# Optimization experiments

Measured on AMD Instinct MI355X. Metric: run time of the kernel, lower is better.

## Reference

```python
import jax, jax.numpy as jnp
import numpy as np
import math

HEAD_DEPTH = 16
CLIP = 10.0
NEG_INF = 1.0e10
# combined scale: (1/sqrt(head_depth)) * log_50(400)
SCALE = (math.log(400.0) / math.log(50.0)) / math.sqrt(HEAD_DEPTH)


def setup_inputs() -> dict:
    key = jax.random.key(0)
    kq, kk, kv, km = jax.random.split(key, 4)
    B, H, S, D = 4, 8, 2048, HEAD_DEPTH
    Q = jax.random.normal(kq, (B, H, S, D), dtype=jnp.float32)
    K = jax.random.normal(kk, (B, H, S, D), dtype=jnp.float32)
    V = jax.random.normal(kv, (B, H, S, D), dtype=jnp.float32)
    # mask: (B, n_nodes, 1) bool; True -> masked (logit set to -inf)
    mask = jax.random.randint(km, (B, S, 1), 0, 2) == 1
    return {"Q": Q, "K": K, "V": V, "mask": mask}


def reference(Q, K, V, mask):
    # logits: (B, H, q_seq, k_seq)
    logits = jnp.einsum("bhqd,bhkd->bhqk", Q, K) * SCALE
    logits = CLIP * jnp.tanh(logits)  # tanh clip
    # mask[:, None, None, :, 0] -> (B, 1, 1, k_seq), True gets -inf
    m = mask[:, None, None, :, 0]
    logits = jnp.where(m, -NEG_INF, logits)
    probs = jax.nn.softmax(logits, axis=-1)
    return jnp.einsum("bhqk,bhkd->bhqd", probs, V)
```

## Files before the change

kernel.cpp:

```cpp
#include <hip/hip_runtime.h>


typedef __fp16 h2 __attribute__((ext_vector_type(2)));
typedef __fp16 h4 __attribute__((ext_vector_type(4)));
typedef float  f4 __attribute__((ext_vector_type(4)));

#define SEQ 2048
#define NBH 32
#define TPB 128
#define KWS_BYTES ((size_t)NBH * TPB * 64 * 8)
#define VWS_BYTES KWS_BYTES
#define BIAS_BYTES ((size_t)4 * SEQ * 4)
#define IDX_BYTES  ((size_t)4 * SEQ * 4)
#define META_BYTES 64
#define WS_NEEDED (KWS_BYTES + VWS_BYTES + BIAS_BYTES + IDX_BYTES + META_BYTES)

__device__ __forceinline__ float fast_exp2(float x) {
#if __has_builtin(__builtin_amdgcn_exp2f)
    return __builtin_amdgcn_exp2f(x);
#else
    return exp2f(x);
#endif
}

__device__ __forceinline__ float dot2acc(h2 a, float accv) {
#if __has_builtin(__builtin_amdgcn_fdot2)
    const h2 one = {(__fp16)1.0f, (__fp16)1.0f};
    return __builtin_amdgcn_fdot2(a, one, accv, false);
#else
    return accv + (float)a[0] + (float)a[1];
#endif
}

__global__ __launch_bounds__(256) void attn_scan(
    const int* __restrict__ maskp, int* __restrict__ idxws,
    float* __restrict__ biasws, int* __restrict__ meta)
{
    __shared__ int partial[256];
    const int b   = blockIdx.x;
    const int tid = threadIdx.x;

    int keep[8], cnt = 0;
    #pragma unroll
    for (int j = 0; j < 8; ++j) {
        keep[j] = (maskp[b * SEQ + tid * 8 + j] == 0);
        cnt += keep[j];
    }
    partial[tid] = cnt;
    __syncthreads();
    for (int off = 1; off < 256; off <<= 1) {
        int add = (tid >= off) ? partial[tid - off] : 0;
        __syncthreads();
        partial[tid] += add;
        __syncthreads();
    }
    const int total = partial[255];
    int pos = partial[tid] - cnt;
    #pragma unroll
    for (int j = 0; j < 8; ++j) {
        if (keep[j]) idxws[b * SEQ + pos++] = tid * 8 + j;
    }
    for (int i = tid; i < SEQ; i += 256) {
        biasws[b * SEQ + i] = (i < total) ? 0.0f : -1.0e30f;
        if (i >= total) idxws[b * SEQ + i] = 0;
    }
    if (tid == 0) {
        int nr = (total + 255) >> 8;
        meta[b] = nr < 1 ? 1 : nr;
    }
}

__global__ __launch_bounds__(256) void attn_prep(
    const float* __restrict__ Kp, const float* __restrict__ Vp,
    const int* __restrict__ idxws,
    __fp16* __restrict__ Kws, __fp16* __restrict__ Vws)
{
    const int tid = threadIdx.x;
    const int T   = blockIdx.x * 4 + (tid >> 6);
    const int l   = tid & 63;
    const int bh  = T >> 7;
    const int t   = T & (TPB - 1);
    const int b   = bh >> 3;
    const int c   = l & 15;
    const int g   = l >> 4;
    const size_t base = (size_t)bh * (SEQ * 16);
    const int*   idx  = idxws + (size_t)b * SEQ;

    {
        const int krow = idx[t * 16 + c];
        f4 kv = *(const f4*)(Kp + base + (size_t)krow * 16 + 4 * g);
        h2 k0 = __builtin_amdgcn_cvt_pkrtz(kv[0], kv[1]);
        h2 k1 = __builtin_amdgcn_cvt_pkrtz(kv[2], kv[3]);
        h4 kh; kh[0] = k0[0]; kh[1] = k0[1]; kh[2] = k1[0]; kh[3] = k1[1];
        *(h4*)(Kws + ((size_t)T * 64 + l) * 4) = kh;
    }
    {
        const int v0 = idx[t * 16 + 4 * g + 0];
        const int v1 = idx[t * 16 + 4 * g + 1];
        const int v2 = idx[t * 16 + 4 * g + 2];
        const int v3 = idx[t * 16 + 4 * g + 3];
        h2 p0 = __builtin_amdgcn_cvt_pkrtz(Vp[base + (size_t)v0 * 16 + c],
                                           Vp[base + (size_t)v1 * 16 + c]);
        h2 p1 = __builtin_amdgcn_cvt_pkrtz(Vp[base + (size_t)v2 * 16 + c],
                                           Vp[base + (size_t)v3 * 16 + c]);
        h4 vh; vh[0] = p0[0]; vh[1] = p0[1]; vh[2] = p1[0]; vh[3] = p1[1];
        *(h4*)(Vws + ((size_t)T * 64 + l) * 4) = vh;
    }
}

__global__ __launch_bounds__(512, 8) void attn_v5(
    const float* __restrict__ Qp, const __fp16* __restrict__ Kws,
    const __fp16* __restrict__ Vws, const float* __restrict__ biasws,
    const int* __restrict__ meta, float* __restrict__ out)
{
    __shared__ __align__(16) _Float16 Kbuf[2][4096];
    __shared__ __align__(16) _Float16 Vbuf[2][4096];
    __shared__ __align__(16) float    Bbuf[2][256];

    const int bid  = blockIdx.x;
    const int bh   = bid >> 5;
    const int qblk = bid & 31;
    const int b    = bh >> 3;
    const int tid  = threadIdx.x;
    const int wave = tid >> 6;
    const int lane = tid & 63;
    const int qt   = wave & 3;
    const int kg   = wave >> 2;
    const int c    = lane & 15;
    const int g    = lane >> 4;

    const size_t base  = (size_t)bh * (SEQ * 16);
    const int    qbase = qblk * 64 + qt * 16;
    const float  c1 = 1.1047809f;
    const float  c2 = -28.8539008f;

    const int nr = meta[b];

    h4 qfrag;
    {
        f4 qv = *(const f4*)(Qp + base + (size_t)(qbase + c) * 16 + 4 * g);
        h2 lo = __builtin_amdgcn_cvt_pkrtz(c1 * qv[0], c1 * qv[1]);
        h2 hi = __builtin_amdgcn_cvt_pkrtz(c1 * qv[2], c1 * qv[3]);
        qfrag[0] = lo[0]; qfrag[1] = lo[1]; qfrag[2] = hi[0]; qfrag[3] = hi[1];
    }

    const f4* ksrc = (const f4*)(Kws + (size_t)bh * TPB * 256);
    const f4* vsrc = (const f4*)(Vws + (size_t)bh * TPB * 256);
    const float* bsrc = biasws + (size_t)b * SEQ;

    f4 kpre = ksrc[tid];
    f4 vpre = vsrc[tid];
    float bpre = (tid < 256) ? bsrc[tid] : 0.0f;
    *(f4*)&Kbuf[0][tid * 8] = kpre;
    *(f4*)&Vbuf[0][tid * 8] = vpre;
    if (tid < 256) Bbuf[0][tid] = bpre;
    {
        const int r1 = (1 < nr) ? 1 : (nr - 1);
        kpre = ksrc[r1 * 512 + tid];
        vpre = vsrc[r1 * 512 + tid];
        if (tid < 256) bpre = bsrc[r1 * 256 + tid];
    }
    __syncthreads();

    f4 acc = {0.f, 0.f, 0.f, 0.f};
    float dsum = 0.f;

    for (int r = 0; r < nr; ++r) {
        const int cb = r & 1, nb = cb ^ 1;
        if (r + 1 < nr) {
            *(f4*)&Kbuf[nb][tid * 8] = kpre;
            *(f4*)&Vbuf[nb][tid * 8] = vpre;
            if (tid < 256) Bbuf[nb][tid] = bpre;
        }
        if (r + 2 < nr) {
            kpre = ksrc[(r + 2) * 512 + tid];
            vpre = vsrc[(r + 2) * 512 + tid];
            if (tid < 256) bpre = bsrc[(r + 2) * 256 + tid];
        }

        const _Float16* Kc = &Kbuf[cb][kg * 2048];
        const _Float16* Vc = &Vbuf[cb][kg * 2048];
        const float*    Bc = &Bbuf[cb][kg * 128];

        #pragma unroll
        for (int t = 0; t < 8; ++t) {
            h4 afrag = *(const h4*)(Kc + t * 256 + lane * 4);
            f4 s = __builtin_amdgcn_mfma_f32_16x16x16f16(
                afrag, qfrag, (f4){0.f, 0.f, 0.f, 0.f}, 0, 0, 0);

            f4 b4 = *(const f4*)(Bc + t * 16 + 4 * g);
            float p[4];
            #pragma unroll
            for (int i = 0; i < 4; ++i) {
                float tt = fast_exp2(s[i]);
                float w  = __builtin_amdgcn_rcpf(1.0f + tt);
                p[i] = fast_exp2(__builtin_fmaf(c2, w, b4[i]));
            }
            h2 plo = __builtin_amdgcn_cvt_pkrtz(p[0], p[1]);
            h2 phi = __builtin_amdgcn_cvt_pkrtz(p[2], p[3]);
            dsum = dot2acc(plo, dsum);
            dsum = dot2acc(phi, dsum);
            h4 pf; pf[0] = plo[0]; pf[1] = plo[1]; pf[2] = phi[0]; pf[3] = phi[1];

            h4 vfrag = *(const h4*)(Vc + t * 256 + lane * 4);
            acc = __builtin_amdgcn_mfma_f32_16x16x16f16(pf, vfrag, acc, 0, 0, 0);
        }
        __syncthreads();
    }

    dsum += __shfl_xor(dsum, 16);
    dsum += __shfl_xor(dsum, 32);

    float* ex = (float*)&Kbuf[0][0];
    const int slot = (qt * 64 + lane) * 5;
    if (kg == 1) {
        ex[slot + 0] = acc[0]; ex[slot + 1] = acc[1];
        ex[slot + 2] = acc[2]; ex[slot + 3] = acc[3];
        ex[slot + 4] = dsum;
    }
    __syncthreads();
    if (kg == 0) {
        const float dT = dsum + ex[slot + 4];
        #pragma unroll
        for (int i = 0; i < 4; ++i) {
            const float denom = __shfl(dT, 4 * g + i);
            out[base + (size_t)(qbase + 4 * g + i) * 16 + c] =
                (acc[i] + ex[slot + i]) / denom;
        }
    }
}

#define KROW 20
#define VROW 520

__global__ __launch_bounds__(512, 8) void attn_fwd_v3(
    const float* __restrict__ Qp, const float* __restrict__ Kp,
    const float* __restrict__ Vp, const int* __restrict__ maskp,
    float* __restrict__ out)
{
    __shared__ __align__(16) _Float16 Klds[512 * KROW];
    __shared__ __align__(16) _Float16 Vt[16 * VROW];
    __shared__ __align__(16) float biasf[512];

    const int bid  = blockIdx.x;
    const int bh   = bid >> 5;
    const int qblk = bid & 31;
    const int b    = bh >> 3;
    const int tid  = threadIdx.x;
    const int wave = tid >> 6;
    const int lane = tid & 63;
    const int qt   = wave & 3;
    const int kg   = wave >> 2;
    const int c    = lane & 15;
    const int g    = lane >> 4;

    const size_t base = (size_t)bh * (SEQ * 16);
    const int qbase = qblk * 64 + qt * 16;
    const float c1 = 1.1047809f;
    const float c2 = -28.8539008f;

    h4 qfrag;
    {
        f4 qv = *(const f4*)(Qp + base + (size_t)(qbase + c) * 16 + 4 * g);
        h2 lo = __builtin_amdgcn_cvt_pkrtz(c1 * qv[0], c1 * qv[1]);
        h2 hi = __builtin_amdgcn_cvt_pkrtz(c1 * qv[2], c1 * qv[3]);
        qfrag[0] = lo[0]; qfrag[1] = lo[1]; qfrag[2] = hi[0]; qfrag[3] = hi[1];
    }

    f4 acc = {0.f, 0.f, 0.f, 0.f};
    float dsum = 0.f;
    const int kgb = kg * 256;

    for (int round = 0; round < 4; ++round) {
        {
            const float* Kc = Kp + base + (size_t)round * (512 * 16);
            const float* Vc = Vp + base + (size_t)round * (512 * 16);
            #pragma unroll
            for (int j = 0; j < 4; ++j) {
                const int i = j * 512 + tid;
                f4 kv = *(const f4*)(Kc + (size_t)i * 4);
                f4 vv = *(const f4*)(Vc + (size_t)i * 4);
                const int key = i >> 2;
                const int dq  = (i & 3) * 4;
                h2 k0 = __builtin_amdgcn_cvt_pkrtz(kv[0], kv[1]);
                h2 k1 = __builtin_amdgcn_cvt_pkrtz(kv[2], kv[3]);
                h4 kh; kh[0] = k0[0]; kh[1] = k0[1]; kh[2] = k1[0]; kh[3] = k1[1];
                *(h4*)&Klds[key * KROW + dq] = kh;
                #pragma unroll
                for (int e = 0; e < 4; ++e)
                    Vt[(dq + e) * VROW + key] = (_Float16)vv[e];
            }
            biasf[tid] = maskp[(size_t)b * SEQ + round * 512 + tid] ? -60.0f : 0.0f;
        }
        __syncthreads();

        #pragma unroll
        for (int t = 0; t < 16; ++t) {
            const int kb = kgb + t * 16;
            h4 afrag = *(const h4*)&Klds[(kb + c) * KROW + 4 * g];
            f4 s = __builtin_amdgcn_mfma_f32_16x16x16f16(
                afrag, qfrag, (f4){0.f, 0.f, 0.f, 0.f}, 0, 0, 0);
            f4 b4 = *(const f4*)&biasf[kb + 4 * g];
            float p[4];
            #pragma unroll
            for (int i = 0; i < 4; ++i) {
                float tt = fast_exp2(s[i]);
                float w  = __builtin_amdgcn_rcpf(1.0f + tt);
                p[i] = fast_exp2(__builtin_fmaf(c2, w, b4[i]));
            }
            h2 plo = __builtin_amdgcn_cvt_pkrtz(p[0], p[1]);
            h2 phi = __builtin_amdgcn_cvt_pkrtz(p[2], p[3]);
            dsum = dot2acc(plo, dsum);
            dsum = dot2acc(phi, dsum);
            h4 pf; pf[0] = plo[0]; pf[1] = plo[1]; pf[2] = phi[0]; pf[3] = phi[1];
            h4 vfrag = *(const h4*)&Vt[c * VROW + kb + 4 * g];
            acc = __builtin_amdgcn_mfma_f32_16x16x16f16(pf, vfrag, acc, 0, 0, 0);
        }
        __syncthreads();
    }

    dsum += __shfl_xor(dsum, 16);
    dsum += __shfl_xor(dsum, 32);

    float* ex = (float*)Klds;
    const int slot = (qt * 64 + lane) * 5;
    if (kg == 1) {
        ex[slot + 0] = acc[0]; ex[slot + 1] = acc[1];
        ex[slot + 2] = acc[2]; ex[slot + 3] = acc[3];
        ex[slot + 4] = dsum;
    }
    __syncthreads();
    if (kg == 0) {
        const float dT = dsum + ex[slot + 4];
        #pragma unroll
        for (int i = 0; i < 4; ++i) {
            const float denom = __shfl(dT, 4 * g + i);
            out[base + (size_t)(qbase + 4 * g + i) * 16 + c] =
                (acc[i] + ex[slot + i]) / denom;
        }
    }
}

extern "C" void kernel_launch(void* const* d_in, const int* in_sizes, int n_in,
                              void* d_out, int out_size, void* d_ws, size_t ws_size,
                              hipStream_t stream) {
    const float* Q    = (const float*)d_in[0];
    const float* K    = (const float*)d_in[1];
    const float* V    = (const float*)d_in[2];
    const int*   mask = (const int*)d_in[3];
    float* out = (float*)d_out;

    if (ws_size >= WS_NEEDED) {
        char* p = (char*)d_ws;
        __fp16* Kws = (__fp16*)p;                       p += KWS_BYTES;
        __fp16* Vws = (__fp16*)p;                       p += VWS_BYTES;
        float*  Bws = (float*)p;                        p += BIAS_BYTES;
        int*    Iws = (int*)p;                          p += IDX_BYTES;
        int*    Mws = (int*)p;
        attn_scan<<<dim3(4), dim3(256), 0, stream>>>(mask, Iws, Bws, Mws);
        attn_prep<<<dim3(1024), dim3(256), 0, stream>>>(K, V, Iws, Kws, Vws);
        attn_v5<<<dim3(1024), dim3(512), 0, stream>>>(Q, Kws, Vws, Bws, Mws, out);
    } else {
        attn_fwd_v3<<<dim3(1024), dim3(512), 0, stream>>>(Q, K, V, mask, out);
    }
}
```

Baseline: 92.77 us.

## Fuse mask compaction and K/V gather into single attention kernel

```diff
diff --git a/kernel.cpp b/kernel.cpp
--- a/kernel.cpp
+++ b/kernel.cpp
@@ -4,16 +4,9 @@
 typedef __fp16 h2 __attribute__((ext_vector_type(2)));
 typedef __fp16 h4 __attribute__((ext_vector_type(4)));
 typedef float  f4 __attribute__((ext_vector_type(4)));
+typedef unsigned short us4 __attribute__((ext_vector_type(4)));
 
 #define SEQ 2048
-#define NBH 32
-#define TPB 128
-#define KWS_BYTES ((size_t)NBH * TPB * 64 * 8)
-#define VWS_BYTES KWS_BYTES
-#define BIAS_BYTES ((size_t)4 * SEQ * 4)
-#define IDX_BYTES  ((size_t)4 * SEQ * 4)
-#define META_BYTES 64
-#define WS_NEEDED (KWS_BYTES + VWS_BYTES + BIAS_BYTES + IDX_BYTES + META_BYTES)
 
 __device__ __forceinline__ float fast_exp2(float x) {
 #if __has_builtin(__builtin_amdgcn_exp2f)
@@ -32,90 +25,15 @@
 #endif
 }
 
-__global__ __launch_bounds__(256) void attn_scan(
-    const int* __restrict__ maskp, int* __restrict__ idxws,
-    float* __restrict__ biasws, int* __restrict__ meta)
-{
-    __shared__ int partial[256];
-    const int b   = blockIdx.x;
-    const int tid = threadIdx.x;
-
-    int keep[8], cnt = 0;
-    #pragma unroll
-    for (int j = 0; j < 8; ++j) {
-        keep[j] = (maskp[b * SEQ + tid * 8 + j] == 0);
-        cnt += keep[j];
-    }
-    partial[tid] = cnt;
-    __syncthreads();
-    for (int off = 1; off < 256; off <<= 1) {
-        int add = (tid >= off) ? partial[tid - off] : 0;
-        __syncthreads();
-        partial[tid] += add;
-        __syncthreads();
-    }
-    const int total = partial[255];
-    int pos = partial[tid] - cnt;
-    #pragma unroll
-    for (int j = 0; j < 8; ++j) {
-        if (keep[j]) idxws[b * SEQ + pos++] = tid * 8 + j;
-    }
-    for (int i = tid; i < SEQ; i += 256) {
-        biasws[b * SEQ + i] = (i < total) ? 0.0f : -1.0e30f;
-        if (i >= total) idxws[b * SEQ + i] = 0;
-    }
-    if (tid == 0) {
-        int nr = (total + 255) >> 8;
-        meta[b] = nr < 1 ? 1 : nr;
-    }
-}
-
-__global__ __launch_bounds__(256) void attn_prep(
-    const float* __restrict__ Kp, const float* __restrict__ Vp,
-    const int* __restrict__ idxws,
-    __fp16* __restrict__ Kws, __fp16* __restrict__ Vws)
-{
-    const int tid = threadIdx.x;
-    const int T   = blockIdx.x * 4 + (tid >> 6);
-    const int l   = tid & 63;
-    const int bh  = T >> 7;
-    const int t   = T & (TPB - 1);
-    const int b   = bh >> 3;
-    const int c   = l & 15;
-    const int g   = l >> 4;
-    const size_t base = (size_t)bh * (SEQ * 16);
-    const int*   idx  = idxws + (size_t)b * SEQ;
-
-    {
-        const int krow = idx[t * 16 + c];
-        f4 kv = *(const f4*)(Kp + base + (size_t)krow * 16 + 4 * g);
-        h2 k0 = __builtin_amdgcn_cvt_pkrtz(kv[0], kv[1]);
-        h2 k1 = __builtin_amdgcn_cvt_pkrtz(kv[2], kv[3]);
-        h4 kh; kh[0] = k0[0]; kh[1] = k0[1]; kh[2] = k1[0]; kh[3] = k1[1];
-        *(h4*)(Kws + ((size_t)T * 64 + l) * 4) = kh;
-    }
-    {
-        const int v0 = idx[t * 16 + 4 * g + 0];
-        const int v1 = idx[t * 16 + 4 * g + 1];
-        const int v2 = idx[t * 16 + 4 * g + 2];
-        const int v3 = idx[t * 16 + 4 * g + 3];
-        h2 p0 = __builtin_amdgcn_cvt_pkrtz(Vp[base + (size_t)v0 * 16 + c],
-                                           Vp[base + (size_t)v1 * 16 + c]);
-        h2 p1 = __builtin_amdgcn_cvt_pkrtz(Vp[base + (size_t)v2 * 16 + c],
-                                           Vp[base + (size_t)v3 * 16 + c]);
-        h4 vh; vh[0] = p0[0]; vh[1] = p0[1]; vh[2] = p1[0]; vh[3] = p1[1];
-        *(h4*)(Vws + ((size_t)T * 64 + l) * 4) = vh;
-    }
-}
-
-__global__ __launch_bounds__(512, 8) void attn_v5(
-    const float* __restrict__ Qp, const __fp16* __restrict__ Kws,
-    const __fp16* __restrict__ Vws, const float* __restrict__ biasws,
-    const int* __restrict__ meta, float* __restrict__ out)
+__global__ __launch_bounds__(512, 8) void attn_fused(
+    const float* __restrict__ Qp, const float* __restrict__ Kp,
+    const float* __restrict__ Vp, const int* __restrict__ maskp,
+    float* __restrict__ out)
 {
     __shared__ __align__(16) _Float16 Kbuf[2][4096];
     __shared__ __align__(16) _Float16 Vbuf[2][4096];
-    __shared__ __align__(16) float    Bbuf[2][256];
+    __shared__ __align__(16) unsigned short idx16[SEQ];
+    __shared__ int wsum[8];
 
     const int bid  = blockIdx.x;
     const int bh   = bid >> 5;
@@ -134,8 +52,6 @@
     const float  c1 = 1.1047809f;
     const float  c2 = -28.8539008f;
 
-    const int nr = meta[b];
-
     h4 qfrag;
     {
         f4 qv = *(const f4*)(Qp + base + (size_t)(qbase + c) * 16 + 4 * g);
@@ -144,21 +60,99 @@
         qfrag[0] = lo[0]; qfrag[1] = lo[1]; qfrag[2] = hi[0]; qfrag[3] = hi[1];
     }
 
-    const f4* ksrc = (const f4*)(Kws + (size_t)bh * TPB * 256);
-    const f4* vsrc = (const f4*)(Vws + (size_t)bh * TPB * 256);
-    const float* bsrc = biasws + (size_t)b * SEQ;
-
-    f4 kpre = ksrc[tid];
-    f4 vpre = vsrc[tid];
-    float bpre = (tid < 256) ? bsrc[tid] : 0.0f;
-    *(f4*)&Kbuf[0][tid * 8] = kpre;
-    *(f4*)&Vbuf[0][tid * 8] = vpre;
-    if (tid < 256) Bbuf[0][tid] = bpre;
+    int4 mv = *(const int4*)(maskp + (size_t)b * SEQ + tid * 4);
+    const int k0 = (mv.x == 0), k1 = (mv.y == 0),
+              k2 = (mv.z == 0), k3 = (mv.w == 0);
+    const int cnt4 = k0 + k1 + k2 + k3;
+    int inc = cnt4;
+    #pragma unroll
+    for (int off = 1; off < 64; off <<= 1) {
+        int v = __shfl_up(inc, off);
+        if (lane >= off) inc += v;
+    }
+    *(us4*)&idx16[tid * 4] = (us4){0, 0, 0, 0};
+    if (lane == 63) wsum[wave] = inc;
+    __syncthreads();
+    int tot = 0, wpre = 0;
+    #pragma unroll
+    for (int w = 0; w < 8; ++w) {
+        int s = wsum[w];
+        if (w < wave) wpre += s;
+        tot += s;
+    }
+    int pos = wpre + inc - cnt4;
+    if (k0) idx16[pos++] = (unsigned short)(tid * 4 + 0);
+    if (k1) idx16[pos++] = (unsigned short)(tid * 4 + 1);
+    if (k2) idx16[pos++] = (unsigned short)(tid * 4 + 2);
+    if (k3) idx16[pos++] = (unsigned short)(tid * 4 + 3);
+    __syncthreads();
+
+    int nr = (tot + 255) >> 8;
+    if (nr == 0) nr = 1;
+
+    const int u  = tid & 31;
+    const int tt = tid >> 5;
+    const int gc = u & 15;
+    const int gh = u >> 4;
+
+    const float* Kb = Kp + base;
+    const float* Vb = Vp + base;
+
+    const int fs0 = (tt * 64 + u)      * 4;
+    const int fs1 = (tt * 64 + u + 32) * 4;
+
+    f4 kA, kB;
+    float vA0, vA1, vA2, vA3, vB0, vB1, vB2, vB3;
+
     {
-        const int r1 = (1 < nr) ? 1 : (nr - 1);
-        kpre = ksrc[r1 * 512 + tid];
-        vpre = vsrc[r1 * 512 + tid];
-        if (tid < 256) bpre = bsrc[r1 * 256 + tid];
+        us4 ra = *(const us4*)&idx16[tt * 16 + 4 * gh];
+        us4 rb = *(const us4*)&idx16[tt * 16 + 4 * gh + 8];
+        const int krow = idx16[tt * 16 + gc];
+        const float* kr = Kb + (size_t)krow * 16;
+        f4 ka_ = *(const f4*)(kr + 4 * gh);
+        f4 kb_ = *(const f4*)(kr + 4 * gh + 8);
+        float a0 = Vb[(size_t)ra[0] * 16 + gc];
+        float a1 = Vb[(size_t)ra[1] * 16 + gc];
+        float a2 = Vb[(size_t)ra[2] * 16 + gc];
+        float a3 = Vb[(size_t)ra[3] * 16 + gc];
+        float b0 = Vb[(size_t)rb[0] * 16 + gc];
+        float b1 = Vb[(size_t)rb[1] * 16 + gc];
+        float b2 = Vb[(size_t)rb[2] * 16 + gc];
+        float b3 = Vb[(size_t)rb[3] * 16 + gc];
+        h2 x0 = __builtin_amdgcn_cvt_pkrtz(ka_[0], ka_[1]);
+        h2 x1 = __builtin_amdgcn_cvt_pkrtz(ka_[2], ka_[3]);
+        h4 kha; kha[0] = x0[0]; kha[1] = x0[1]; kha[2] = x1[0]; kha[3] = x1[1];
+        *(h4*)&Kbuf[0][fs0] = kha;
+        h2 y0 = __builtin_amdgcn_cvt_pkrtz(kb_[0], kb_[1]);
+        h2 y1 = __builtin_amdgcn_cvt_pkrtz(kb_[2], kb_[3]);
+        h4 khb; khb[0] = y0[0]; khb[1] = y0[1]; khb[2] = y1[0]; khb[3] = y1[1];
+        *(h4*)&Kbuf[0][fs1] = khb;
+        h2 p0 = __builtin_amdgcn_cvt_pkrtz(a0, a1);
+        h2 p1 = __builtin_amdgcn_cvt_pkrtz(a2, a3);
+        h4 vha; vha[0] = p0[0]; vha[1] = p0[1]; vha[2] = p1[0]; vha[3] = p1[1];
+        *(h4*)&Vbuf[0][fs0] = vha;
+        h2 q0 = __builtin_amdgcn_cvt_pkrtz(b0, b1);
+        h2 q1 = __builtin_amdgcn_cvt_pkrtz(b2, b3);
+        h4 vhb; vhb[0] = q0[0]; vhb[1] = q0[1]; vhb[2] = q1[0]; vhb[3] = q1[1];
+        *(h4*)&Vbuf[0][fs1] = vhb;
+    }
+    {
+        const int r1 = (nr > 1) ? 1 : 0;
+        const int ib = r1 * 256 + tt * 16;
+        us4 ra = *(const us4*)&idx16[ib + 4 * gh];
+        us4 rb = *(const us4*)&idx16[ib + 4 * gh + 8];
+        const int krow = idx16[ib + gc];
+        const float* kr = Kb + (size_t)krow * 16;
+        kA = *(const f4*)(kr + 4 * gh);
+        kB = *(const f4*)(kr + 4 * gh + 8);
+        vA0 = Vb[(size_t)ra[0] * 16 + gc];
+        vA1 = Vb[(size_t)ra[1] * 16 + gc];
+        vA2 = Vb[(size_t)ra[2] * 16 + gc];
+        vA3 = Vb[(size_t)ra[3] * 16 + gc];
+        vB0 = Vb[(size_t)rb[0] * 16 + gc];
+        vB1 = Vb[(size_t)rb[1] * 16 + gc];
+        vB2 = Vb[(size_t)rb[2] * 16 + gc];
+        vB3 = Vb[(size_t)rb[3] * 16 + gc];
     }
     __syncthreads();
 
@@ -168,19 +162,44 @@
     for (int r = 0; r < nr; ++r) {
         const int cb = r & 1, nb = cb ^ 1;
         if (r + 1 < nr) {
-            *(f4*)&Kbuf[nb][tid * 8] = kpre;
-            *(f4*)&Vbuf[nb][tid * 8] = vpre;
-            if (tid < 256) Bbuf[nb][tid] = bpre;
+            h2 x0 = __builtin_amdgcn_cvt_pkrtz(kA[0], kA[1]);
+            h2 x1 = __builtin_amdgcn_cvt_pkrtz(kA[2], kA[3]);
+            h4 kha; kha[0] = x0[0]; kha[1] = x0[1]; kha[2] = x1[0]; kha[3] = x1[1];
+            *(h4*)&Kbuf[nb][fs0] = kha;
+            h2 y0 = __builtin_amdgcn_cvt_pkrtz(kB[0], kB[1]);
+            h2 y1 = __builtin_amdgcn_cvt_pkrtz(kB[2], kB[3]);
+            h4 khb; khb[0] = y0[0]; khb[1] = y0[1]; khb[2] = y1[0]; khb[3] = y1[1];
+            *(h4*)&Kbuf[nb][fs1] = khb;
+            h2 p0 = __builtin_amdgcn_cvt_pkrtz(vA0, vA1);
+            h2 p1 = __builtin_amdgcn_cvt_pkrtz(vA2, vA3);
+            h4 vha; vha[0] = p0[0]; vha[1] = p0[1]; vha[2] = p1[0]; vha[3] = p1[1];
+            *(h4*)&Vbuf[nb][fs0] = vha;
+            h2 q0 = __builtin_amdgcn_cvt_pkrtz(vB0, vB1);
+            h2 q1 = __builtin_amdgcn_cvt_pkrtz(vB2, vB3);
+            h4 vhb; vhb[0] = q0[0]; vhb[1] = q0[1]; vhb[2] = q1[0]; vhb[3] = q1[1];
+            *(h4*)&Vbuf[nb][fs1] = vhb;
         }
         if (r + 2 < nr) {
-            kpre = ksrc[(r + 2) * 512 + tid];
-            vpre = vsrc[(r + 2) * 512 + tid];
-            if (tid < 256) bpre = bsrc[(r + 2) * 256 + tid];
+            const int ib = (r + 2) * 256 + tt * 16;
+            us4 ra = *(const us4*)&idx16[ib + 4 * gh];
+            us4 rb = *(const us4*)&idx16[ib + 4 * gh + 8];
+            const int krow = idx16[ib + gc];
+            const float* kr = Kb + (size_t)krow * 16;
+            kA = *(const f4*)(kr + 4 * gh);
+            kB = *(const f4*)(kr + 4 * gh + 8);
+            vA0 = Vb[(size_t)ra[0] * 16 + gc];
+            vA1 = Vb[(size_t)ra[1] * 16 + gc];
+            vA2 = Vb[(size_t)ra[2] * 16 + gc];
+            vA3 = Vb[(size_t)ra[3] * 16 + gc];
+            vB0 = Vb[(size_t)rb[0] * 16 + gc];
+            vB1 = Vb[(size_t)rb[1] * 16 + gc];
+            vB2 = Vb[(size_t)rb[2] * 16 + gc];
+            vB3 = Vb[(size_t)rb[3] * 16 + gc];
         }
 
         const _Float16* Kc = &Kbuf[cb][kg * 2048];
         const _Float16* Vc = &Vbuf[cb][kg * 2048];
-        const float*    Bc = &Bbuf[cb][kg * 128];
+        const int lim = tot - r * 256 - kg * 128 - 4 * g;
 
         #pragma unroll
         for (int t = 0; t < 8; ++t) {
@@ -188,13 +207,13 @@
             f4 s = __builtin_amdgcn_mfma_f32_16x16x16f16(
                 afrag, qfrag, (f4){0.f, 0.f, 0.f, 0.f}, 0, 0, 0);
 
-            f4 b4 = *(const f4*)(Bc + t * 16 + 4 * g);
             float p[4];
             #pragma unroll
             for (int i = 0; i < 4; ++i) {
-                float tt = fast_exp2(s[i]);
-                float w  = __builtin_amdgcn_rcpf(1.0f + tt);
-                p[i] = fast_exp2(__builtin_fmaf(c2, w, b4[i]));
+                float tv = fast_exp2(s[i]);
+                float w  = __builtin_amdgcn_rcpf(1.0f + tv);
+                float bsel = (t * 16 + i < lim) ? 0.0f : -1.0e30f;
+                p[i] = fast_exp2(__builtin_fmaf(c2, w, bsel));
             }
             h2 plo = __builtin_amdgcn_cvt_pkrtz(p[0], p[1]);
             h2 phi = __builtin_amdgcn_cvt_pkrtz(p[2], p[3]);
@@ -212,117 +231,6 @@
     dsum += __shfl_xor(dsum, 32);
 
     float* ex = (float*)&Kbuf[0][0];
-    const int slot = (qt * 64 + lane) * 5;
-    if (kg == 1) {
-        ex[slot + 0] = acc[0]; ex[slot + 1] = acc[1];
-        ex[slot + 2] = acc[2]; ex[slot + 3] = acc[3];
-        ex[slot + 4] = dsum;
-    }
-    __syncthreads();
-    if (kg == 0) {
-        const float dT = dsum + ex[slot + 4];
-        #pragma unroll
-        for (int i = 0; i < 4; ++i) {
-            const float denom = __shfl(dT, 4 * g + i);
-            out[base + (size_t)(qbase + 4 * g + i) * 16 + c] =
-                (acc[i] + ex[slot + i]) / denom;
-        }
-    }
-}
-
-#define KROW 20
-#define VROW 520
-
-__global__ __launch_bounds__(512, 8) void attn_fwd_v3(
-    const float* __restrict__ Qp, const float* __restrict__ Kp,
-    const float* __restrict__ Vp, const int* __restrict__ maskp,
-    float* __restrict__ out)
-{
-    __shared__ __align__(16) _Float16 Klds[512 * KROW];
-    __shared__ __align__(16) _Float16 Vt[16 * VROW];
-    __shared__ __align__(16) float biasf[512];
-
-    const int bid  = blockIdx.x;
-    const int bh   = bid >> 5;
-    const int qblk = bid & 31;
-    const int b    = bh >> 3;
-    const int tid  = threadIdx.x;
-    const int wave = tid >> 6;
-    const int lane = tid & 63;
-    const int qt   = wave & 3;
-    const int kg   = wave >> 2;
-    const int c    = lane & 15;
-    const int g    = lane >> 4;
-
-    const size_t base = (size_t)bh * (SEQ * 16);
-    const int qbase = qblk * 64 + qt * 16;
-    const float c1 = 1.1047809f;
-    const float c2 = -28.8539008f;
-
-    h4 qfrag;
-    {
-        f4 qv = *(const f4*)(Qp + base + (size_t)(qbase + c) * 16 + 4 * g);
-        h2 lo = __builtin_amdgcn_cvt_pkrtz(c1 * qv[0], c1 * qv[1]);
-        h2 hi = __builtin_amdgcn_cvt_pkrtz(c1 * qv[2], c1 * qv[3]);
-        qfrag[0] = lo[0]; qfrag[1] = lo[1]; qfrag[2] = hi[0]; qfrag[3] = hi[1];
-    }
-
-    f4 acc = {0.f, 0.f, 0.f, 0.f};
-    float dsum = 0.f;
-    const int kgb = kg * 256;
-
-    for (int round = 0; round < 4; ++round) {
-        {
-            const float* Kc = Kp + base + (size_t)round * (512 * 16);
-            const float* Vc = Vp + base + (size_t)round * (512 * 16);
-            #pragma unroll
-            for (int j = 0; j < 4; ++j) {
-                const int i = j * 512 + tid;
-                f4 kv = *(const f4*)(Kc + (size_t)i * 4);
-                f4 vv = *(const f4*)(Vc + (size_t)i * 4);
-                const int key = i >> 2;
-                const int dq  = (i & 3) * 4;
-                h2 k0 = __builtin_amdgcn_cvt_pkrtz(kv[0], kv[1]);
-                h2 k1 = __builtin_amdgcn_cvt_pkrtz(kv[2], kv[3]);
-                h4 kh; kh[0] = k0[0]; kh[1] = k0[1]; kh[2] = k1[0]; kh[3] = k1[1];
-                *(h4*)&Klds[key * KROW + dq] = kh;
-                #pragma unroll
-                for (int e = 0; e < 4; ++e)
-                    Vt[(dq + e) * VROW + key] = (_Float16)vv[e];
-            }
-            biasf[tid] = maskp[(size_t)b * SEQ + round * 512 + tid] ? -60.0f : 0.0f;
-        }
-        __syncthreads();
-
-        #pragma unroll
-        for (int t = 0; t < 16; ++t) {
-            const int kb = kgb + t * 16;
-            h4 afrag = *(const h4*)&Klds[(kb + c) * KROW + 4 * g];
-            f4 s = __builtin_amdgcn_mfma_f32_16x16x16f16(
-                afrag, qfrag, (f4){0.f, 0.f, 0.f, 0.f}, 0, 0, 0);
-            f4 b4 = *(const f4*)&biasf[kb + 4 * g];
-            float p[4];
-            #pragma unroll
-            for (int i = 0; i < 4; ++i) {
-                float tt = fast_exp2(s[i]);
-                float w  = __builtin_amdgcn_rcpf(1.0f + tt);
-                p[i] = fast_exp2(__builtin_fmaf(c2, w, b4[i]));
-            }
-            h2 plo = __builtin_amdgcn_cvt_pkrtz(p[0], p[1]);
-            h2 phi = __builtin_amdgcn_cvt_pkrtz(p[2], p[3]);
-            dsum = dot2acc(plo, dsum);
-            dsum = dot2acc(phi, dsum);
-            h4 pf; pf[0] = plo[0]; pf[1] = plo[1]; pf[2] = phi[0]; pf[3] = phi[1];
-            h4 vfrag = *(const h4*)&Vt[c * VROW + kb + 4 * g];
-            acc = __builtin_amdgcn_mfma_f32_16x16x16f16(pf, vfrag, acc, 0, 0, 0);
-        }
-        __syncthreads();
-    }
-
-    dsum += __shfl_xor(dsum, 16);
-    dsum += __shfl_xor(dsum, 32);
-
-    float* ex = (float*)Klds;
     const int slot = (qt * 64 + lane) * 5;
     if (kg == 1) {
         ex[slot + 0] = acc[0]; ex[slot + 1] = acc[1];
@@ -349,18 +257,5 @@
     const float* V    = (const float*)d_in[2];
     const int*   mask = (const int*)d_in[3];
     float* out = (float*)d_out;
-
-    if (ws_size >= WS_NEEDED) {
-        char* p = (char*)d_ws;
-        __fp16* Kws = (__fp16*)p;                       p += KWS_BYTES;
-        __fp16* Vws = (__fp16*)p;                       p += VWS_BYTES;
-        float*  Bws = (float*)p;                        p += BIAS_BYTES;
-        int*    Iws = (int*)p;                          p += IDX_BYTES;
-        int*    Mws = (int*)p;
-        attn_scan<<<dim3(4), dim3(256), 0, stream>>>(mask, Iws, Bws, Mws);
-        attn_prep<<<dim3(1024), dim3(256), 0, stream>>>(K, V, Iws, Kws, Vws);
-        attn_v5<<<dim3(1024), dim3(512), 0, stream>>>(Q, Kws, Vws, Bws, Mws, out);
-    } else {
-        attn_fwd_v3<<<dim3(1024), dim3(512), 0, stream>>>(Q, K, V, mask, out);
-    }
-}
+    attn_fused<<<dim3(1024), dim3(512), 0, stream>>>(Q, K, V, mask, out);
+}
```

Result: no change. 94.12 us (+1.4%).
